# Performance work log

Hardware: AMD Instinct MI355X
Metric: run time of the kernel (lower is better)

Reference implementation:

```python
import jax, jax.numpy as jnp
import numpy as np

V, E, H, N, T, L = 32000, 1024, 1024, 64, 32, 196


def setup_inputs() -> dict:
    key = jax.random.key(0)
    ks = jax.random.split(key, 12)
    s = 0.02
    return {
        "inputs": jax.random.randint(ks[0], (N, T), 0, V, dtype=jnp.int32),
        "img_features": jax.random.normal(ks[1], (N, L, H), dtype=jnp.float32),
        "emb": jax.random.normal(ks[2], (V, E), dtype=jnp.float32) * s,
        "w_ih1": jax.random.normal(ks[3], (4 * H, E), dtype=jnp.float32) * s,
        "w_hh1": jax.random.normal(ks[4], (4 * H, H), dtype=jnp.float32) * s,
        "b_ih1": jax.random.normal(ks[5], (4 * H,), dtype=jnp.float32) * s,
        "b_hh1": jax.random.normal(ks[6], (4 * H,), dtype=jnp.float32) * s,
        "w_ih2": jax.random.normal(ks[7], (4 * H, 2 * H), dtype=jnp.float32) * s,
        "w_hh2": jax.random.normal(ks[8], (4 * H, H), dtype=jnp.float32) * s,
        "b_ih2": jax.random.normal(ks[9], (4 * H,), dtype=jnp.float32) * s,
        "b_hh2": jax.random.normal(ks[10], (4 * H,), dtype=jnp.float32) * s,
    }


def _lstm_cell(x, h, c, w_ih, w_hh, b_ih, b_hh):
    # PyTorch LSTMCell: gates ordered i, f, g, o
    g = x @ w_ih.T + b_ih + h @ w_hh.T + b_hh
    i, f, gg, o = jnp.split(g, 4, axis=-1)
    c_new = jax.nn.sigmoid(f) * c + jax.nn.sigmoid(i) * jnp.tanh(gg)
    h_new = jax.nn.sigmoid(o) * jnp.tanh(c_new)
    return h_new, c_new


def reference(inputs, img_features, emb, w_ih1, w_hh1, b_ih1, b_hh1,
              w_ih2, w_hh2, b_ih2, b_hh2):
    n, t = inputs.shape
    hdim = w_hh1.shape[1]
    embedded = emb[inputs]                      # (N, T, E)
    # faithful to original: .view(T, N, -1) is a reshape, NOT a transpose
    xs = embedded.reshape(t, n, -1)             # (T, N, E)

    def step(carry, x_t):
        h1, c1, h2, c2 = carry
        h1, c1 = _lstm_cell(x_t, h1, c1, w_ih1, w_hh1, b_ih1, b_hh1)
        # attention: raw dot-product weights (no softmax in original)
        alpha = jnp.einsum('nd,nld->nl', h1, img_features)   # (N, L)
        v_att = jnp.einsum('nl,nld->nd', alpha, img_features) # (N, D)
        x2 = jnp.concatenate([v_att, h1], axis=1)             # (N, 2H)
        h2, c2 = _lstm_cell(x2, h2, c2, w_ih2, w_hh2, b_ih2, b_hh2)
        return (h1, c1, h2, c2), h2

    zeros = jnp.zeros((n, hdim), dtype=img_features.dtype)
    init = (zeros, zeros, zeros, zeros)
    _, hs = jax.lax.scan(step, init, xs)        # (T, N, H)
    # faithful to original: cat along dim 0 then .view(N, T, -1) == reshape
    return hs.reshape(n, t, -1)
```

## Files before the change

kernel.cpp:

```cpp
#include <hip/hip_runtime.h>
#include <math.h>

typedef __attribute__((ext_vector_type(8))) short bf16x8;
typedef __attribute__((ext_vector_type(4))) short short4v;
typedef __attribute__((ext_vector_type(4))) float f32x4;

__device__ __forceinline__ float sigm(float x) { return 1.f / (1.f + expf(-x)); }

__device__ __forceinline__ float bf2f(short x) {
    unsigned u = ((unsigned)(unsigned short)x) << 16;
    float f; __builtin_memcpy(&f, &u, 4); return f;
}
__device__ __forceinline__ short f2bf(float f) {
    unsigned u; __builtin_memcpy(&u, &f, 4);
    unsigned r = (u + 0x7fffu + ((u >> 16) & 1u)) >> 16;
    return (short)r;
}

__device__ __forceinline__ unsigned sys_ld(const unsigned* p) {
    return __hip_atomic_load(p, __ATOMIC_RELAXED, __HIP_MEMORY_SCOPE_SYSTEM);
}
__device__ __forceinline__ void sys_st(unsigned* p, unsigned v) {
    __hip_atomic_store(p, v, __ATOMIC_RELAXED, __HIP_MEMORY_SCOPE_SYSTEM);
}

#define OFF_C1      0u
#define OFF_C2      262144u
#define OFF_H1HI    786432u
#define OFF_H1LO    5111808u
#define OFF_H1F     9437184u
#define OFF_X0HI    17825792u
#define OFF_X0LO    22020096u
#define OFF_B1      26214400u
#define OFF_B2      26230784u
#define OFF_WHH1HI  26247168u
#define OFF_WHH1LO  34635776u
#define OFF_WIH1HI  43024384u
#define OFF_WIH1LO  51412992u
#define OFF_WHH2HI  59801600u
#define OFF_WVHI    68190208u
#define OFF_WVLO    76578816u
#define OFF_WH2HI   84967424u
#define OFF_X12     93356032u

__global__ __launch_bounds__(256) void zero_ws(float4* __restrict__ p) {
    int i = blockIdx.x * 256 + threadIdx.x;
    p[i] = make_float4(0.f, 0.f, 0.f, 0.f);
}

__global__ __launch_bounds__(256) void zero_slots(unsigned* __restrict__ p) {
    int i = blockIdx.x * 256 + threadIdx.x;
    __hip_atomic_store(p + i, 0u, __ATOMIC_RELAXED, __HIP_MEMORY_SCOPE_SYSTEM);
}

__global__ __launch_bounds__(256) void perm_w_split(const float* __restrict__ src,
                                                    short* __restrict__ hi,
                                                    short* __restrict__ lo,
                                                    int rs, int co) {
    int idx = blockIdx.x * 256 + threadIdx.x;
    int jp = idx >> 8;
    int kq = idx & 255;
    int jsrc = (jp & 3) * 1024 + (jp >> 2);
    float4 v = *(const float4*)(src + (size_t)jsrc * rs + co + kq * 4);
    float a[4] = {v.x, v.y, v.z, v.w};
    short4v h, l;
    #pragma unroll
    for (int e = 0; e < 4; e++) {
        short q = f2bf(a[e]);
        h[e] = q;
        l[e] = f2bf(a[e] - bf2f(q));
    }
    *(short4v*)(hi + (size_t)jp * 1024 + kq * 4) = h;
    *(short4v*)(lo + (size_t)jp * 1024 + kq * 4) = l;
}

__global__ __launch_bounds__(256) void bias_prep(
    const float* __restrict__ bi1, const float* __restrict__ bh1,
    const float* __restrict__ bi2, const float* __restrict__ bh2,
    float* __restrict__ b1p, float* __restrict__ b2p) {
    int jp = blockIdx.x * 256 + threadIdx.x;
    int j = (jp & 3) * 1024 + (jp >> 2);
    b1p[jp] = bi1[j] + bh1[j];
    b2p[jp] = bi2[j] + bh2[j];
}

__global__ __launch_bounds__(256) void gather_x0_split(
    const int* __restrict__ tokens, const float* __restrict__ emb,
    short* __restrict__ hi, short* __restrict__ lo) {
    int idx = blockIdx.x * 256 + threadIdx.x;
    int p = idx >> 8;
    int k0 = (idx & 255) * 4;
    int tok = tokens[p];
    float4 v = *(const float4*)(emb + (size_t)tok * 1024 + k0);
    float a[4] = {v.x, v.y, v.z, v.w};
    short4v h, l;
    #pragma unroll
    for (int e = 0; e < 4; e++) {
        short q = f2bf(a[e]);
        h[e] = q;
        l[e] = f2bf(a[e] - bf2f(q));
    }
    *(short4v*)(hi + (size_t)p * 1024 + k0) = h;
    *(short4v*)(lo + (size_t)p * 1024 + k0) = l;
}

__global__ __launch_bounds__(256) void big_gemm(
    const short* __restrict__ A0, const short* __restrict__ A1s,
    const short* __restrict__ A2s, const short* __restrict__ A3s,
    const short* __restrict__ B0, const short* __restrict__ B1s,
    const short* __restrict__ B2s, const short* __restrict__ B3s,
    const float* __restrict__ bias, float* __restrict__ C, int K) {
    __shared__ short As[128 * 40];
    __shared__ short Bs[128 * 40];
    int tid = threadIdx.x;
    int n0 = blockIdx.x * 128;
    int m0 = blockIdx.y * 128;
    int lane = tid & 63, w = tid >> 6;
    int wm = (w >> 1) * 64, wn = (w & 1) * 64;
    int quad = lane >> 4, l16 = lane & 15;
    int srow = tid >> 2;
    int skc = (tid & 3) * 8;

    f32x4 acc[4][4];
    f32x4 z4 = {0.f, 0.f, 0.f, 0.f};
    #pragma unroll
    for (int i = 0; i < 4; i++)
        #pragma unroll
        for (int j = 0; j < 4; j++) acc[i][j] = z4;

    for (int k0 = 0; k0 < K; k0 += 32) {
        int seg = k0 >> 10;
        const short* Ab = (seg == 0) ? A0 : (seg == 1) ? A1s : (seg == 2) ? A2s : A3s;
        const short* Bb = (seg == 0) ? B0 : (seg == 1) ? B1s : (seg == 2) ? B2s : B3s;
        int kk = (k0 & 1023) + skc;
        const short* ga = Ab + (size_t)(m0 + srow) * 1024 + kk;
        const short* gb = Bb + (size_t)(n0 + srow) * 1024 + kk;
        bf16x8 av0 = *(const bf16x8*)ga;
        bf16x8 av1 = *(const bf16x8*)(ga + 64 * 1024);
        bf16x8 bv0 = *(const bf16x8*)gb;
        bf16x8 bv1 = *(const bf16x8*)(gb + 64 * 1024);
        __syncthreads();
        *(bf16x8*)&As[srow * 40 + skc] = av0;
        *(bf16x8*)&As[(srow + 64) * 40 + skc] = av1;
        *(bf16x8*)&Bs[srow * 40 + skc] = bv0;
        *(bf16x8*)&Bs[(srow + 64) * 40 + skc] = bv1;
        __syncthreads();
        bf16x8 af[4], bfr[4];
        #pragma unroll
        for (int im = 0; im < 4; im++)
            af[im] = *(const bf16x8*)&As[(wm + im * 16 + l16) * 40 + quad * 8];
        #pragma unroll
        for (int in = 0; in < 4; in++)
            bfr[in] = *(const bf16x8*)&Bs[(wn + in * 16 + l16) * 40 + quad * 8];
        #pragma unroll
        for (int im = 0; im < 4; im++)
            #pragma unroll
            for (int in = 0; in < 4; in++)
                acc[im][in] = __builtin_amdgcn_mfma_f32_16x16x32_bf16(
                    af[im], bfr[in], acc[im][in], 0, 0, 0);
    }
    #pragma unroll
    for (int in = 0; in < 4; in++) {
        int j = n0 + wn + in * 16 + l16;
        float bsv = bias[j];
        #pragma unroll
        for (int im = 0; im < 4; im++) {
            #pragma unroll
            for (int r = 0; r < 4; r++) {
                int p = m0 + wm + im * 16 + quad * 4 + r;
                C[(size_t)p * 4096 + j] = acc[im][in][r] + bsv;
            }
        }
    }
}

__global__ __launch_bounds__(256, 1) void lstm1_fused(
    const short* __restrict__ Whi, const short* __restrict__ Wlo,
    const float* __restrict__ X12,
    short* __restrict__ H1hi, short* __restrict__ H1lo,
    float* __restrict__ H1f,
    unsigned* __restrict__ arrive, unsigned* __restrict__ release) {
    __shared__ short wsh[16 * 1032];
    __shared__ float red[4 * 64 * 16];

    int tid = threadIdx.x;
    int lane = tid & 63, w = tid >> 6;
    int quad = lane >> 4, l16 = lane & 15;
    int g = blockIdx.x;
    int kbase = w * 256;

    for (int i = tid; i < 2048; i += 256) {
        int r = i >> 7;
        int k = (i & 127) * 8;
        *(bf16x8*)&wsh[r * 1032 + k] =
            *(const bf16x8*)(Whi + (size_t)(g * 16 + r) * 1024 + k);
    }

    int s = tid >> 2, dl = tid & 3;
    int d = g * 4 + dl;
    float creg = 0.f;

    __syncthreads();

    const short* bhp = &wsh[l16 * 1032 + kbase + quad * 8];
    const short* blp = Wlo + (size_t)(g * 16 + l16) * 1024 + kbase + quad * 8;
    const float* xgp = X12 + (size_t)s * 4096 + g * 16 + dl * 4;

    float4 xg = *(const float4*)xgp;

    for (int t = 0; t < 32; t++) {
        f32x4 acc[4];
        f32x4 z4 = {0.f, 0.f, 0.f, 0.f};
        acc[0] = z4; acc[1] = z4; acc[2] = z4; acc[3] = z4;

        if (t > 0) {
            const short* ah = H1hi + (size_t)t * 65536 + (size_t)l16 * 1024 + kbase + quad * 8;
            const short* al = H1lo + (size_t)t * 65536 + (size_t)l16 * 1024 + kbase + quad * 8;
            #pragma unroll
            for (int i = 0; i < 8; i++) {
                int k = i * 32;
                bf16x8 Bh = *(const bf16x8*)(bhp + k);
                bf16x8 Bl = *(const bf16x8*)(blp + k);
                #pragma unroll
                for (int mt = 0; mt < 4; mt++) {
                    bf16x8 Ah = *(const bf16x8*)(ah + mt * 16 * 1024 + k);
                    bf16x8 Al = *(const bf16x8*)(al + mt * 16 * 1024 + k);
                    acc[mt] = __builtin_amdgcn_mfma_f32_16x16x32_bf16(Ah, Bh, acc[mt], 0, 0, 0);
                    acc[mt] = __builtin_amdgcn_mfma_f32_16x16x32_bf16(Al, Bh, acc[mt], 0, 0, 0);
                    acc[mt] = __builtin_amdgcn_mfma_f32_16x16x32_bf16(Ah, Bl, acc[mt], 0, 0, 0);
                }
            }
        }
        #pragma unroll
        for (int mt = 0; mt < 4; mt++)
            #pragma unroll
            for (int r = 0; r < 4; r++) {
                int sr = mt * 16 + quad * 4 + r;
                red[(w * 64 + sr) * 16 + l16] = acc[mt][r];
            }
        __syncthreads();

        float gi = 0.f, gf = 0.f, gg = 0.f, go = 0.f;
        #pragma unroll
        for (int w2 = 0; w2 < 4; w2++) {
            const float* rp = &red[(w2 * 64 + s) * 16 + dl * 4];
            gi += rp[0]; gf += rp[1]; gg += rp[2]; go += rp[3];
        }
        gi += xg.x; gf += xg.y; gg += xg.z; go += xg.w;
        float cn = sigm(gf) * creg + sigm(gi) * tanhf(gg);
        creg = cn;
        float hn = sigm(go) * tanhf(cn);
        short q = f2bf(hn);
        short ql = f2bf(hn - bf2f(q));
        __hip_atomic_store(&H1hi[(size_t)(t + 1) * 65536 + s * 1024 + d], q,
                           __ATOMIC_RELAXED, __HIP_MEMORY_SCOPE_AGENT);
        __hip_atomic_store(&H1lo[(size_t)(t + 1) * 65536 + s * 1024 + d], ql,
                           __ATOMIC_RELAXED, __HIP_MEMORY_SCOPE_AGENT);
        __syncthreads();
        if (t != 31) {
            unsigned tgt = (unsigned)(t + 1);
            if (tid == 0) sys_st(arrive + (size_t)g * 32, tgt);
            H1f[(size_t)t * 65536 + s * 1024 + d] = hn;
            xg = *(const float4*)(xgp + (size_t)(t + 1) * 262144);
            if (g == 0) {
                unsigned* my = arrive + (size_t)tid * 32;
                while (sys_ld(my) < tgt) __builtin_amdgcn_s_sleep(2);
                __syncthreads();
                if (tid == 0) sys_st(release, tgt);
            } else {
                if (tid == 0)
                    while (sys_ld(release) < tgt) __builtin_amdgcn_s_sleep(2);
                __syncthreads();
            }
            asm volatile("" ::: "memory");
        } else {
            H1f[(size_t)t * 65536 + s * 1024 + d] = hn;
        }
    }
}

__global__ __launch_bounds__(256, 1) void lstm2_fused(
    const short* __restrict__ W, const float* __restrict__ X12,
    short* __restrict__ H2,
    float* __restrict__ out,
    unsigned* __restrict__ arrive, unsigned* __restrict__ release) {
    __shared__ short wsh[16 * 1032];
    __shared__ float red[4 * 64 * 16];

    int tid = threadIdx.x;
    int lane = tid & 63, w = tid >> 6;
    int quad = lane >> 4, l16 = lane & 15;
    int g = blockIdx.x;
    int kbase = w * 256;

    for (int i = tid; i < 2048; i += 256) {
        int r = i >> 7;
        int k = (i & 127) * 8;
        *(bf16x8*)&wsh[r * 1032 + k] =
            *(const bf16x8*)(W + (size_t)(g * 16 + r) * 1024 + k);
    }

    int s = tid >> 2, dl = tid & 3;
    int d = g * 4 + dl;
    float creg = 0.f;

    __syncthreads();

    const short* bp = &wsh[l16 * 1032 + kbase + quad * 8];
    const float* xgp = X12 + (size_t)s * 4096 + g * 16 + dl * 4;

    float4 xg = *(const float4*)xgp;

    for (int t = 0; t < 32; t++) {
        f32x4 acc[4];
        f32x4 z4 = {0.f, 0.f, 0.f, 0.f};
        acc[0] = z4; acc[1] = z4; acc[2] = z4; acc[3] = z4;

        if (t > 0) {
            const short* ar = H2 + (size_t)t * 65536 + (size_t)l16 * 1024 + kbase + quad * 8;
            #pragma unroll
            for (int i = 0; i < 8; i++) {
                int k = i * 32;
                bf16x8 b = *(const bf16x8*)(bp + k);
                #pragma unroll
                for (int mt = 0; mt < 4; mt++) {
                    bf16x8 a = *(const bf16x8*)(ar + mt * 16 * 1024 + k);
                    acc[mt] = __builtin_amdgcn_mfma_f32_16x16x32_bf16(a, b, acc[mt], 0, 0, 0);
                }
            }
        }
        #pragma unroll
        for (int mt = 0; mt < 4; mt++)
            #pragma unroll
            for (int r = 0; r < 4; r++) {
                int sr = mt * 16 + quad * 4 + r;
                red[(w * 64 + sr) * 16 + l16] = acc[mt][r];
            }
        __syncthreads();

        float gi = 0.f, gf = 0.f, gg = 0.f, go = 0.f;
        #pragma unroll
        for (int w2 = 0; w2 < 4; w2++) {
            const float* rp = &red[(w2 * 64 + s) * 16 + dl * 4];
            gi += rp[0]; gf += rp[1]; gg += rp[2]; go += rp[3];
        }
        gi += xg.x; gf += xg.y; gg += xg.z; go += xg.w;
        float cn = sigm(gf) * creg + sigm(gi) * tanhf(gg);
        creg = cn;
        float hn = sigm(go) * tanhf(cn);
        __hip_atomic_store(&H2[(size_t)(t + 1) * 65536 + s * 1024 + d], f2bf(hn),
                           __ATOMIC_RELAXED, __HIP_MEMORY_SCOPE_AGENT);
        __syncthreads();
        if (t != 31) {
            unsigned tgt = (unsigned)(t + 1);
            if (tid == 0) sys_st(arrive + (size_t)g * 32, tgt);
            out[(size_t)t * 65536 + s * 1024 + d] = hn;
            xg = *(const float4*)(xgp + (size_t)(t + 1) * 262144);
            if (g == 0) {
                unsigned* my = arrive + (size_t)tid * 32;
                while (sys_ld(my) < tgt) __builtin_amdgcn_s_sleep(2);
                __syncthreads();
                if (tid == 0) sys_st(release, tgt);
            } else {
                if (tid == 0)
                    while (sys_ld(release) < tgt) __builtin_amdgcn_s_sleep(2);
                __syncthreads();
            }
            asm volatile("" ::: "memory");
        } else {
            out[(size_t)t * 65536 + s * 1024 + d] = hn;
        }
    }
}

__global__ __launch_bounds__(256) void attn_batch(
    const float* __restrict__ H1f, const float* __restrict__ F,
    short* __restrict__ Vhi, short* __restrict__ Vlo) {
    __shared__ float vs[4][4][1024];
    int n = blockIdx.x, tg = blockIdx.y;
    int tid = threadIdx.x, lane = tid & 63, w = tid >> 6;

    float h[4][16];
    #pragma unroll
    for (int tt = 0; tt < 4; tt++) {
        const float* hp = H1f + ((size_t)((tg * 4 + tt) * 64 + n)) * 1024 + lane * 16;
        #pragma unroll
        for (int j = 0; j < 4; j++) {
            float4 v = *(const float4*)(hp + j * 4);
            h[tt][j * 4 + 0] = v.x; h[tt][j * 4 + 1] = v.y;
            h[tt][j * 4 + 2] = v.z; h[tt][j * 4 + 3] = v.w;
        }
    }
    float vacc[4][16];
    #pragma unroll
    for (int tt = 0; tt < 4; tt++)
        #pragma unroll
        for (int j = 0; j < 16; j++) vacc[tt][j] = 0.f;

    const float* Fn = F + ((size_t)n * 196) * 1024 + lane * 16;
    for (int l = w; l < 196; l += 4) {
        const float* fr = Fn + (size_t)l * 1024;
        float f[16];
        #pragma unroll
        for (int j = 0; j < 4; j++) {
            float4 v = *(const float4*)(fr + j * 4);
            f[j * 4 + 0] = v.x; f[j * 4 + 1] = v.y;
            f[j * 4 + 2] = v.z; f[j * 4 + 3] = v.w;
        }
        float p[4] = {0.f, 0.f, 0.f, 0.f};
        #pragma unroll
        for (int tt = 0; tt < 4; tt++)
            #pragma unroll
            for (int j = 0; j < 16; j++) p[tt] += f[j] * h[tt][j];
        #pragma unroll
        for (int off = 32; off > 0; off >>= 1) {
            #pragma unroll
            for (int tt = 0; tt < 4; tt++) p[tt] += __shfl_xor(p[tt], off, 64);
        }
        #pragma unroll
        for (int tt = 0; tt < 4; tt++)
            #pragma unroll
            for (int j = 0; j < 16; j++) vacc[tt][j] += p[tt] * f[j];
    }
    #pragma unroll
    for (int tt = 0; tt < 4; tt++)
        #pragma unroll
        for (int j4 = 0; j4 < 4; j4++) {
            float4 v;
            v.x = vacc[tt][j4 * 4 + 0]; v.y = vacc[tt][j4 * 4 + 1];
            v.z = vacc[tt][j4 * 4 + 2]; v.w = vacc[tt][j4 * 4 + 3];
            *(float4*)&vs[w][tt][lane * 16 + j4 * 4] = v;
        }
    __syncthreads();
    int d0 = tid * 4;
    #pragma unroll
    for (int tt = 0; tt < 4; tt++) {
        float4 a = *(const float4*)&vs[0][tt][d0];
        float4 b = *(const float4*)&vs[1][tt][d0];
        float4 cc = *(const float4*)&vs[2][tt][d0];
        float4 e = *(const float4*)&vs[3][tt][d0];
        float sv[4];
        sv[0] = a.x + b.x + cc.x + e.x;
        sv[1] = a.y + b.y + cc.y + e.y;
        sv[2] = a.z + b.z + cc.z + e.z;
        sv[3] = a.w + b.w + cc.w + e.w;
        short4v b1, b2;
        #pragma unroll
        for (int e2 = 0; e2 < 4; e2++) {
            short q = f2bf(sv[e2]);
            b1[e2] = q;
            b2[e2] = f2bf(sv[e2] - bf2f(q));
        }
        size_t row = ((size_t)(tg * 4 + tt) * 64 + n) * 1024 + d0;
        *(short4v*)(Vhi + row) = b1;
        *(short4v*)(Vlo + row) = b2;
    }
}

extern "C" void kernel_launch(void* const* d_in, const int* in_sizes, int n_in,
                              void* d_out, int out_size, void* d_ws, size_t ws_size,
                              hipStream_t stream) {
    const int*   tokens = (const int*)d_in[0];
    const float* imgf   = (const float*)d_in[1];
    const float* emb    = (const float*)d_in[2];
    const float* w_ih1  = (const float*)d_in[3];
    const float* w_hh1  = (const float*)d_in[4];
    const float* b_ih1  = (const float*)d_in[5];
    const float* b_hh1  = (const float*)d_in[6];
    const float* w_ih2  = (const float*)d_in[7];
    const float* w_hh2  = (const float*)d_in[8];
    const float* b_ih2  = (const float*)d_in[9];
    const float* b_hh2  = (const float*)d_in[10];
    float* out = (float*)d_out;
    char* ws = (char*)d_ws;

    unsigned* arrive1  = (unsigned*)(ws + OFF_C1);
    unsigned* release1 = (unsigned*)(ws + OFF_C1 + 32768u);
    unsigned* arrive2  = (unsigned*)(ws + OFF_C1 + 65536u);
    unsigned* release2 = (unsigned*)(ws + OFF_C1 + 98304u);
    short* H1hi   = (short*)(ws + OFF_H1HI);
    short* H1lo   = (short*)(ws + OFF_H1LO);
    float* H1f    = (float*)(ws + OFF_H1F);
    short* H2     = (short*)(ws + OFF_H1F);
    short* X0hi   = (short*)(ws + OFF_X0HI);
    short* X0lo   = (short*)(ws + OFF_X0LO);
    short* Vhi    = (short*)(ws + OFF_X0HI);
    short* Vlo    = (short*)(ws + OFF_X0LO);
    float* bias1p = (float*)(ws + OFF_B1);
    float* bias2p = (float*)(ws + OFF_B2);
    short* whh1hi = (short*)(ws + OFF_WHH1HI);
    short* whh1lo = (short*)(ws + OFF_WHH1LO);
    short* wih1hi = (short*)(ws + OFF_WIH1HI);
    short* wih1lo = (short*)(ws + OFF_WIH1LO);
    short* whh2hi = (short*)(ws + OFF_WHH2HI);
    short* wvhi   = (short*)(ws + OFF_WVHI);
    short* wvlo   = (short*)(ws + OFF_WVLO);
    short* wh2hi  = (short*)(ws + OFF_WH2HI);
    float* X12    = (float*)(ws + OFF_X12);
    short* dump   = (short*)(ws + OFF_X12);

    zero_slots<<<128, 256, 0, stream>>>((unsigned*)(ws + OFF_C1));
    perm_w_split<<<4096, 256, 0, stream>>>(w_hh1, whh1hi, whh1lo, 1024, 0);
    perm_w_split<<<4096, 256, 0, stream>>>(w_ih1, wih1hi, wih1lo, 1024, 0);
    perm_w_split<<<4096, 256, 0, stream>>>(w_hh2, whh2hi, dump, 1024, 0);
    perm_w_split<<<4096, 256, 0, stream>>>(w_ih2, wvhi, wvlo, 2048, 0);
    perm_w_split<<<4096, 256, 0, stream>>>(w_ih2, wh2hi, dump, 2048, 1024);
    bias_prep<<<16, 256, 0, stream>>>(b_ih1, b_hh1, b_ih2, b_hh2, bias1p, bias2p);
    gather_x0_split<<<2048, 256, 0, stream>>>(tokens, emb, X0hi, X0lo);

    big_gemm<<<dim3(32, 16), 256, 0, stream>>>(
        X0hi, X0lo, X0hi, X0hi,
        wih1hi, wih1hi, wih1lo, wih1hi,
        bias1p, X12, 3072);

    lstm1_fused<<<256, 256, 0, stream>>>(
        whh1hi, whh1lo, X12, H1hi, H1lo, H1f, arrive1, release1);

    attn_batch<<<dim3(64, 8), 256, 0, stream>>>(H1f, imgf, Vhi, Vlo);

    big_gemm<<<dim3(32, 16), 256, 0, stream>>>(
        Vhi, Vlo, Vhi, H1hi + 65536,
        wvhi, wvhi, wvlo, wh2hi,
        bias2p, X12, 4096);

    lstm2_fused<<<256, 256, 0, stream>>>(
        whh2hi, X12, H2, out, arrive2, release2);
}
```

Measured before the change: 1.043 ms.

## Replace centralized grid barrier with distributed polling and pack h stores

Result: slower. 1.143 ms (+9.6%).

```diff
diff --git a/kernel.cpp b/kernel.cpp
--- a/kernel.cpp
+++ b/kernel.cpp
@@ -25,7 +25,6 @@
 }
 
 #define OFF_C1      0u
-#define OFF_C2      262144u
 #define OFF_H1HI    786432u
 #define OFF_H1LO    5111808u
 #define OFF_H1F     9437184u
@@ -179,7 +178,7 @@
     const float* __restrict__ X12,
     short* __restrict__ H1hi, short* __restrict__ H1lo,
     float* __restrict__ H1f,
-    unsigned* __restrict__ arrive, unsigned* __restrict__ release) {
+    unsigned* __restrict__ arrive) {
     __shared__ short wsh[16 * 1032];
     __shared__ float red[4 * 64 * 16];
 
@@ -252,26 +251,49 @@
         float hn = sigm(go) * tanhf(cn);
         short q = f2bf(hn);
         short ql = f2bf(hn - bf2f(q));
-        __hip_atomic_store(&H1hi[(size_t)(t + 1) * 65536 + s * 1024 + d], q,
-                           __ATOMIC_RELAXED, __HIP_MEMORY_SCOPE_AGENT);
-        __hip_atomic_store(&H1lo[(size_t)(t + 1) * 65536 + s * 1024 + d], ql,
-                           __ATOMIC_RELAXED, __HIP_MEMORY_SCOPE_AGENT);
+
+        unsigned pr = ((unsigned)(unsigned short)q) |
+                      (((unsigned)(unsigned short)ql) << 16);
+        int lb = lane & ~3;
+        unsigned p0 = __shfl(pr, lb + 0, 64);
+        unsigned p1 = __shfl(pr, lb + 1, 64);
+        unsigned p2 = __shfl(pr, lb + 2, 64);
+        unsigned p3 = __shfl(pr, lb + 3, 64);
+        if (dl == 0) {
+            unsigned long long hi4 =
+                (unsigned long long)(p0 & 0xffffu) |
+                ((unsigned long long)(p1 & 0xffffu) << 16) |
+                ((unsigned long long)(p2 & 0xffffu) << 32) |
+                ((unsigned long long)(p3 & 0xffffu) << 48);
+            unsigned long long lo4 =
+                (unsigned long long)(p0 >> 16) |
+                ((unsigned long long)(p1 >> 16) << 16) |
+                ((unsigned long long)(p2 >> 16) << 32) |
+                ((unsigned long long)(p3 >> 16) << 48);
+            __hip_atomic_store(
+                (unsigned long long*)&H1hi[(size_t)(t + 1) * 65536 + s * 1024 + g * 4],
+                hi4, __ATOMIC_RELAXED, __HIP_MEMORY_SCOPE_AGENT);
+            __hip_atomic_store(
+                (unsigned long long*)&H1lo[(size_t)(t + 1) * 65536 + s * 1024 + g * 4],
+                lo4, __ATOMIC_RELAXED, __HIP_MEMORY_SCOPE_AGENT);
+        }
         __syncthreads();
         if (t != 31) {
             unsigned tgt = (unsigned)(t + 1);
-            if (tid == 0) sys_st(arrive + (size_t)g * 32, tgt);
+            if (tid == 0) sys_st(arrive + g, tgt);
             H1f[(size_t)t * 65536 + s * 1024 + d] = hn;
             xg = *(const float4*)(xgp + (size_t)(t + 1) * 262144);
-            if (g == 0) {
-                unsigned* my = arrive + (size_t)tid * 32;
-                while (sys_ld(my) < tgt) __builtin_amdgcn_s_sleep(2);
-                __syncthreads();
-                if (tid == 0) sys_st(release, tgt);
-            } else {
-                if (tid == 0)
-                    while (sys_ld(release) < tgt) __builtin_amdgcn_s_sleep(2);
-                __syncthreads();
-            }
+            if (tid < 64) {
+                const unsigned* p = arrive + tid * 4;
+                for (;;) {
+                    unsigned a = sys_ld(p + 0), b = sys_ld(p + 1);
+                    unsigned c = sys_ld(p + 2), e = sys_ld(p + 3);
+                    int ok = (a >= tgt) && (b >= tgt) && (c >= tgt) && (e >= tgt);
+                    if (__all(ok)) break;
+                    __builtin_amdgcn_s_sleep(4);
+                }
+            }
+            __syncthreads();
             asm volatile("" ::: "memory");
         } else {
             H1f[(size_t)t * 65536 + s * 1024 + d] = hn;
@@ -283,7 +305,7 @@
     const short* __restrict__ W, const float* __restrict__ X12,
     short* __restrict__ H2,
     float* __restrict__ out,
-    unsigned* __restrict__ arrive, unsigned* __restrict__ release) {
+    unsigned* __restrict__ arrive) {
     __shared__ short wsh[16 * 1032];
     __shared__ float red[4 * 64 * 16];
 
@@ -348,24 +370,40 @@
         float cn = sigm(gf) * creg + sigm(gi) * tanhf(gg);
         creg = cn;
         float hn = sigm(go) * tanhf(cn);
-        __hip_atomic_store(&H2[(size_t)(t + 1) * 65536 + s * 1024 + d], f2bf(hn),
-                           __ATOMIC_RELAXED, __HIP_MEMORY_SCOPE_AGENT);
+
+        unsigned pr = (unsigned)(unsigned short)f2bf(hn);
+        int lb = lane & ~3;
+        unsigned p0 = __shfl(pr, lb + 0, 64);
+        unsigned p1 = __shfl(pr, lb + 1, 64);
+        unsigned p2 = __shfl(pr, lb + 2, 64);
+        unsigned p3 = __shfl(pr, lb + 3, 64);
+        if (dl == 0) {
+            unsigned long long h4 =
+                (unsigned long long)(p0 & 0xffffu) |
+                ((unsigned long long)(p1 & 0xffffu) << 16) |
+                ((unsigned long long)(p2 & 0xffffu) << 32) |
+                ((unsigned long long)(p3 & 0xffffu) << 48);
+            __hip_atomic_store(
+                (unsigned long long*)&H2[(size_t)(t + 1) * 65536 + s * 1024 + g * 4],
+                h4, __ATOMIC_RELAXED, __HIP_MEMORY_SCOPE_AGENT);
+        }
         __syncthreads();
         if (t != 31) {
             unsigned tgt = (unsigned)(t + 1);
-            if (tid == 0) sys_st(arrive + (size_t)g * 32, tgt);
+            if (tid == 0) sys_st(arrive + g, tgt);
             out[(size_t)t * 65536 + s * 1024 + d] = hn;
             xg = *(const float4*)(xgp + (size_t)(t + 1) * 262144);
-            if (g == 0) {
-                unsigned* my = arrive + (size_t)tid * 32;
-                while (sys_ld(my) < tgt) __builtin_amdgcn_s_sleep(2);
-                __syncthreads();
-                if (tid == 0) sys_st(release, tgt);
-            } else {
-                if (tid == 0)
-                    while (sys_ld(release) < tgt) __builtin_amdgcn_s_sleep(2);
-                __syncthreads();
-            }
+            if (tid < 64) {
+                const unsigned* p = arrive + tid * 4;
+                for (;;) {
+                    unsigned a = sys_ld(p + 0), b = sys_ld(p + 1);
+                    unsigned c = sys_ld(p + 2), e = sys_ld(p + 3);
+                    int ok = (a >= tgt) && (b >= tgt) && (c >= tgt) && (e >= tgt);
+                    if (__all(ok)) break;
+                    __builtin_amdgcn_s_sleep(4);
+                }
+            }
+            __syncthreads();
             asm volatile("" ::: "memory");
         } else {
             out[(size_t)t * 65536 + s * 1024 + d] = hn;
@@ -474,10 +512,8 @@
     float* out = (float*)d_out;
     char* ws = (char*)d_ws;
 
-    unsigned* arrive1  = (unsigned*)(ws + OFF_C1);
-    unsigned* release1 = (unsigned*)(ws + OFF_C1 + 32768u);
-    unsigned* arrive2  = (unsigned*)(ws + OFF_C1 + 65536u);
-    unsigned* release2 = (unsigned*)(ws + OFF_C1 + 98304u);
+    unsigned* arrive1 = (unsigned*)(ws + OFF_C1);
+    unsigned* arrive2 = (unsigned*)(ws + OFF_C1 + 4096u);
     short* H1hi   = (short*)(ws + OFF_H1HI);
     short* H1lo   = (short*)(ws + OFF_H1LO);
     float* H1f    = (float*)(ws + OFF_H1F);
@@ -499,7 +535,7 @@
     float* X12    = (float*)(ws + OFF_X12);
     short* dump   = (short*)(ws + OFF_X12);
 
-    zero_slots<<<128, 256, 0, stream>>>((unsigned*)(ws + OFF_C1));
+    zero_slots<<<8, 256, 0, stream>>>((unsigned*)(ws + OFF_C1));
     perm_w_split<<<4096, 256, 0, stream>>>(w_hh1, whh1hi, whh1lo, 1024, 0);
     perm_w_split<<<4096, 256, 0, stream>>>(w_ih1, wih1hi, wih1lo, 1024, 0);
     perm_w_split<<<4096, 256, 0, stream>>>(w_hh2, whh2hi, dump, 1024, 0);
@@ -514,7 +550,7 @@
         bias1p, X12, 3072);
 
     lstm1_fused<<<256, 256, 0, stream>>>(
-        whh1hi, whh1lo, X12, H1hi, H1lo, H1f, arrive1, release1);
+        whh1hi, whh1lo, X12, H1hi, H1lo, H1f, arrive1);
 
     attn_batch<<<dim3(64, 8), 256, 0, stream>>>(H1f, imgf, Vhi, Vlo);
 
@@ -524,5 +560,5 @@
         bias2p, X12, 4096);
 
     lstm2_fused<<<256, 256, 0, stream>>>(
-        whh2hi, X12, H2, out, arrive2, release2);
-}
+        whh2hi, X12, H2, out, arrive2);
+}
```
